# Optimization experiments

Hardware: AMD Instinct MI355X
Metric: run time of the kernel (lower is better)

Reference implementation:

```python
import math
import jax, jax.numpy as jnp
import numpy as np

B, V, D, H, DE, DFF = 2, 2048, 1024, 16, 256, 4096
DK = D // H


def setup_inputs() -> dict:
    key = jax.random.key(0)
    ks = jax.random.split(key, 24)
    n = lambda k, shape, s=0.02: (jax.random.normal(k, shape, jnp.float32) * s)
    z = lambda *shape: jnp.zeros(shape, jnp.float32)
    return {
        'x': jax.random.normal(ks[0], (B, V, D), jnp.float32),
        'e_node': jax.random.normal(ks[1], (B, V, DE), jnp.float32),
        'conn': jax.random.uniform(ks[2], (B, V, V), jnp.float32),
        'ln1_g': jnp.ones((D,), jnp.float32), 'ln1_b': z(D),
        'f1w1': n(ks[3], (DE, 2 * D)), 'f1b1': z(2 * D),
        'f1w2': n(ks[4], (2 * D, 2 * D)), 'f1b2': z(2 * D),
        'wq': n(ks[5], (D, D)), 'bq': z(D),
        'wk': n(ks[6], (D, D)), 'bk': z(D),
        'wv': n(ks[7], (D, D)), 'bv': z(D),
        'wp': n(ks[8], (D, D)), 'bp': z(D),
        'ln2_g': jnp.ones((D,), jnp.float32), 'ln2_b': z(D),
        'f2w1': n(ks[9], (DE, 2 * D)), 'f2b1': z(2 * D),
        'f2w2': n(ks[10], (2 * D, 2 * D)), 'f2b2': z(2 * D),
        'ffw1': n(ks[11], (D, DFF)), 'ffb1': z(DFF),
        'ffw2': n(ks[12], (DFF, D)), 'ffb2': z(D),
    }


def _ln(x, g, b):
    m = x.mean(-1, keepdims=True)
    v = ((x - m) ** 2).mean(-1, keepdims=True)
    return (x - m) / jnp.sqrt(v + 1e-5) * g + b


def _film(e, w1, b1, w2, b2):
    h = jax.nn.gelu(e @ w1 + b1, approximate=False)  # torch F.gelu default = exact erf
    gb = h @ w2 + b2
    return jnp.split(gb, 2, axis=-1)  # gamma, beta


def reference(x, e_node, conn, ln1_g, ln1_b, f1w1, f1b1, f1w2, f1b2,
              wq, bq, wk, bk, wv, bv, wp, bp, ln2_g, ln2_b,
              f2w1, f2b1, f2w2, f2b2, ffw1, ffb1, ffw2, ffb2):
    b, v, d = x.shape
    # Pre-norm + FiLM 1
    y = _ln(x, ln1_g, ln1_b)
    g1, be1 = _film(e_node, f1w1, f1b1, f1w2, f1b2)
    y = y * (1.0 + g1) + be1
    # Multi-head attention with additive log(conn) mask
    heads = lambda t: t.reshape(b, v, H, DK).transpose(0, 2, 1, 3)  # [B,h,V,dk]
    Q = heads(y @ wq + bq)
    K = heads(y @ wk + bk)
    Vv = heads(y @ wv + bv)
    logits = jnp.einsum('bhqd,bhkd->bhqk', Q, K) / math.sqrt(DK)
    log_mask = jnp.log(jnp.clip(conn, 0.0, 1.0) + 1e-6)[:, None]  # [B,1,V,V]
    s = logits + log_mask
    s = s - s.max(-1, keepdims=True)
    a = jnp.exp(s)
    a = a / (a.sum(-1, keepdims=True) + 1e-8)
    o = jnp.einsum('bhqk,bhkd->bhqd', a, Vv)
    o = o.transpose(0, 2, 1, 3).reshape(b, v, d)
    x = x + (o @ wp + bp)
    # Pre-norm + FiLM 2 + FFN
    y2 = _ln(x, ln2_g, ln2_b)
    g2, be2 = _film(e_node, f2w1, f2b1, f2w2, f2b2)
    y2 = y2 * (1.0 + g2) + be2
    y2 = jax.nn.gelu(y2 @ ffw1 + ffb1, approximate=False) @ ffw2 + ffb2
    return x + y2
```

## Files before the change

kernel.cpp:

```cpp
#include <hip/hip_runtime.h>
#include <math.h>
#include <stdint.h>

#define B_   2
#define V_   2048
#define D_   1024
#define H_   16
#define DK_  64
#define DE_  256
#define DFF_ 4096
#define M_   (B_*V_)
#define D2_  (2*D_)
#define D3_  (3*D_)

typedef unsigned short u16;
typedef unsigned int   u32;
typedef __bf16 bf16x8 __attribute__((ext_vector_type(8)));
typedef u16    u16x8  __attribute__((ext_vector_type(8)));
typedef u16    u16x4  __attribute__((ext_vector_type(4)));
typedef float  f32x4  __attribute__((ext_vector_type(4)));
typedef u32    u32x2  __attribute__((ext_vector_type(2)));
typedef u32    u32x4  __attribute__((ext_vector_type(4)));

__device__ __forceinline__ float bf2f(u16 u) {
    union { unsigned int i; float f; } z; z.i = ((unsigned int)u) << 16; return z.f;
}
__device__ __forceinline__ u16 f2bf(float f) {
    union { float f; unsigned int i; } z; z.f = f;
    unsigned int x = z.i;
    return (u16)((x + 0x7fffu + ((x >> 16) & 1u)) >> 16);
}
__device__ __forceinline__ float gelu_erf(float v) {
    return 0.5f * v * (1.0f + erff(v * 0.70710678118654752f));
}
__device__ __forceinline__ float ldv(const float* p) { return *p; }
__device__ __forceinline__ float ldv(const u16* p)   { return bf2f(*p); }
__device__ __forceinline__ void  stv(float* p, float v) { *p = v; }
__device__ __forceinline__ void  stv(u16* p,   float v) { *p = f2bf(v); }

__device__ __forceinline__ void gload16(const u16* g, u16* lds)
{
    __builtin_amdgcn_global_load_lds(
        (const __attribute__((address_space(1))) void*)g,
        (__attribute__((address_space(3))) void*)(uintptr_t)lds,
        16, 0, 0);
}

__device__ __forceinline__ void barrier_raw()
{
    asm volatile("" ::: "memory");
    __builtin_amdgcn_s_barrier();
    asm volatile("" ::: "memory");
}

__global__ void convT_k(const float* __restrict__ W, u16* __restrict__ Wt, int K, int N)
{
    __shared__ float tile[32][33];
    const int n0 = blockIdx.x * 32, k0 = blockIdx.y * 32;
    const int tx = threadIdx.x, ty = threadIdx.y;
    #pragma unroll
    for (int j = 0; j < 4; ++j)
        tile[ty * 4 + j][tx] = W[(size_t)(k0 + ty * 4 + j) * N + n0 + tx];
    __syncthreads();
    #pragma unroll
    for (int j = 0; j < 4; ++j)
        Wt[(size_t)(n0 + ty * 4 + j) * K + k0 + tx] = f2bf(tile[tx][ty * 4 + j]);
}

__global__ void convT3_k(const float* __restrict__ W0, const float* __restrict__ W1,
                         const float* __restrict__ W2, u16* __restrict__ Wt)
{
    __shared__ float tile[32][33];
    const float* W = blockIdx.z == 0 ? W0 : (blockIdx.z == 1 ? W1 : W2);
    u16* dst = Wt + (size_t)blockIdx.z * D_ * D_;
    const int n0 = blockIdx.x * 32, k0 = blockIdx.y * 32;
    const int tx = threadIdx.x, ty = threadIdx.y;
    #pragma unroll
    for (int j = 0; j < 4; ++j)
        tile[ty * 4 + j][tx] = W[(size_t)(k0 + ty * 4 + j) * D_ + n0 + tx];
    __syncthreads();
    #pragma unroll
    for (int j = 0; j < 4; ++j)
        dst[(size_t)(n0 + ty * 4 + j) * D_ + k0 + tx] = f2bf(tile[tx][ty * 4 + j]);
}

__global__ void conv_k(const float* __restrict__ X, u16* __restrict__ Y)
{
    const int i = (blockIdx.x * 256 + threadIdx.x) * 4;
    f32x4 v = *reinterpret_cast<const f32x4*>(X + i);
    u16x4 o;
    #pragma unroll
    for (int j = 0; j < 4; ++j) o[j] = f2bf(v[j]);
    *reinterpret_cast<u16x4*>(Y + i) = o;
}

__global__ void lmask_k(const float* __restrict__ conn, u16* __restrict__ Lm)
{
    const size_t i = ((size_t)blockIdx.x * 256 + threadIdx.x) * 8;
    f32x4 a = *reinterpret_cast<const f32x4*>(conn + i);
    f32x4 b = *reinterpret_cast<const f32x4*>(conn + i + 4);
    u16x8 o;
    #pragma unroll
    for (int j = 0; j < 4; ++j) {
        o[j]     = f2bf(__log2f(fminf(fmaxf(a[j], 0.f), 1.f) + 1e-6f));
        o[j + 4] = f2bf(__log2f(fminf(fmaxf(b[j], 0.f), 1.f) + 1e-6f));
    }
    *reinterpret_cast<u16x8*>(Lm + i) = o;
}

__global__ void qkvbias_k(const float* __restrict__ bq, const float* __restrict__ bk,
                          const float* __restrict__ bv, float* __restrict__ o)
{
    int i = blockIdx.x * 256 + threadIdx.x;
    o[i] = i < 1024 ? bq[i] : (i < 2048 ? bk[i - 1024] : bv[i - 2048]);
}

template<typename TX>
__launch_bounds__(256)
__global__ void xstats_k(const TX* __restrict__ X, float* __restrict__ stats)
{
    const int row = blockIdx.x;
    const int tid = threadIdx.x;
    const TX* xr = X + (size_t)row * D_ + tid * 4;
    float s = 0.f, sq = 0.f;
    if constexpr (sizeof(TX) == 4) {
        f32x4 v4 = *reinterpret_cast<const f32x4*>(xr);
        #pragma unroll
        for (int j = 0; j < 4; ++j) { s += v4[j]; sq += v4[j] * v4[j]; }
    } else {
        u16x4 v4 = *reinterpret_cast<const u16x4*>(xr);
        #pragma unroll
        for (int j = 0; j < 4; ++j) { float v = bf2f(v4[j]); s += v; sq += v * v; }
    }
    #pragma unroll
    for (int off = 32; off; off >>= 1) {
        s  += __shfl_xor(s, off);
        sq += __shfl_xor(sq, off);
    }
    __shared__ float rs[4], rq[4];
    const int w = tid >> 6;
    if ((tid & 63) == 0) { rs[w] = s; rq[w] = sq; }
    __syncthreads();
    if (tid == 0) {
        s  = rs[0] + rs[1] + rs[2] + rs[3];
        sq = rq[0] + rq[1] + rq[2] + rq[3];
        float mean = s * (1.0f / D_);
        float var  = sq * (1.0f / D_) - mean * mean;
        stats[row * 2]     = mean;
        stats[row * 2 + 1] = rsqrtf(fmaxf(var, 0.f) + 1e-5f);
    }
}

template<int EPI, int BN, typename TC, typename TRES>
__launch_bounds__(256)
__global__ void gemm_k(const u16* __restrict__ A, const u16* __restrict__ Wt,
                       const float* __restrict__ bias, const TRES* __restrict__ res,
                       TC* __restrict__ C, int M, int N, int K)
{
    constexpr int NB = BN / 32;
    constexpr int IB = BN / 32;
    __shared__ u16 As[2][128 * 64];
    __shared__ u16 Bs[2][BN * 64];

    const int tid  = threadIdx.x;
    const int lane = tid & 63;
    const int w    = tid >> 6;
    const int wm   = (w >> 1) * 64, wn = (w & 1) * (BN / 2);
    const int m0   = blockIdx.y * 128, n0 = blockIdx.x * BN;
    const int l15  = lane & 15, l4 = lane >> 4;
    const int rStage = lane >> 3;

    int rrA[4], ccA[4];
    #pragma unroll
    for (int i = 0; i < 4; ++i) {
        rrA[i] = w * 32 + i * 8 + rStage;
        ccA[i] = (lane & 7) ^ (rrA[i] & 7);
    }
    int rrB[IB], ccB[IB];
    #pragma unroll
    for (int i = 0; i < IB; ++i) {
        rrB[i] = w * (BN / 4) + i * 8 + rStage;
        ccB[i] = (lane & 7) ^ (rrB[i] & 7);
    }

    auto stage = [&](int kt, int dd) {
        const int k0 = kt * 64;
        #pragma unroll
        for (int i = 0; i < 4; ++i)
            gload16(A + (size_t)(m0 + rrA[i]) * K + k0 + ccA[i] * 8, &As[dd][w * 2048 + i * 512]);
        #pragma unroll
        for (int i = 0; i < IB; ++i)
            gload16(Wt + (size_t)(n0 + rrB[i]) * K + k0 + ccB[i] * 8, &Bs[dd][w * (BN * 16) + i * 512]);
    };

    f32x4 acc[4][NB] = {};
    const int NT = K / 64;

    stage(0, 0);

    for (int t = 0; t < NT; ++t) {
        const int d = t & 1;
        barrier_raw();
        if (t + 1 < NT) {
            stage(t + 1, d ^ 1);
            if constexpr (BN == 128) asm volatile("s_waitcnt vmcnt(8)" ::: "memory");
            else                     asm volatile("s_waitcnt vmcnt(6)" ::: "memory");
        } else {
            asm volatile("s_waitcnt vmcnt(0)" ::: "memory");
        }
        barrier_raw();
        __builtin_amdgcn_sched_barrier(0);

        #pragma unroll
        for (int kk = 0; kk < 2; ++kk) {
            bf16x8 a[4], b[NB];
            #pragma unroll
            for (int mb = 0; mb < 4; ++mb) {
                int r  = wm + mb * 16 + l15;
                int ph = (kk * 4 + l4) ^ (r & 7);
                a[mb] = *reinterpret_cast<const bf16x8*>(&As[d][r * 64 + ph * 8]);
            }
            #pragma unroll
            for (int nb = 0; nb < NB; ++nb) {
                int r  = wn + nb * 16 + l15;
                int ph = (kk * 4 + l4) ^ (r & 7);
                b[nb] = *reinterpret_cast<const bf16x8*>(&Bs[d][r * 64 + ph * 8]);
            }
            #pragma unroll
            for (int mb = 0; mb < 4; ++mb)
                #pragma unroll
                for (int nb = 0; nb < NB; ++nb)
                    acc[mb][nb] = __builtin_amdgcn_mfma_f32_16x16x32_bf16(a[mb], b[nb], acc[mb][nb], 0, 0, 0);
        }
    }

    #pragma unroll
    for (int nb = 0; nb < NB; ++nb) {
        int col = n0 + wn + nb * 16 + l15;
        float bv = bias[col];
        #pragma unroll
        for (int mb = 0; mb < 4; ++mb) {
            #pragma unroll
            for (int i = 0; i < 4; ++i) {
                int row = m0 + wm + mb * 16 + l4 * 4 + i;
                float v = acc[mb][nb][i] + bv;
                if (EPI == 1) v = gelu_erf(v);
                if (EPI == 2) v += ldv(res + (size_t)row * N + col);
                stv(C + (size_t)row * N + col, v);
            }
        }
    }
}

template<typename TX>
__launch_bounds__(256)
__global__ void gemmfilm_k(const u16* __restrict__ A, const u16* __restrict__ Wt,
                           const float* __restrict__ b2, const TX* __restrict__ X,
                           const float* __restrict__ stats,
                           const float* __restrict__ lng, const float* __restrict__ lnb,
                           u16* __restrict__ Y)
{
    constexpr int Kc = D2_;
    __shared__ u16 As[2][128 * 64];
    __shared__ u16 Bs[2][128 * 64];

    const int tid  = threadIdx.x;
    const int lane = tid & 63;
    const int w    = tid >> 6;
    const int wm   = (w >> 1) * 64, wn = (w & 1) * 32;
    const int m0   = blockIdx.y * 128, n0 = blockIdx.x * 64;
    const int l15  = lane & 15, l4 = lane >> 4;
    const int rStage = lane >> 3;

    int rrA[4], ccA[4];
    #pragma unroll
    for (int i = 0; i < 4; ++i) {
        rrA[i] = w * 32 + i * 8 + rStage;
        ccA[i] = (lane & 7) ^ (rrA[i] & 7);
    }
    int rowB[4], ccB[4], grB[4];
    #pragma unroll
    for (int i = 0; i < 4; ++i) {
        int lr = w * 16 + (i & 1) * 8 + rStage;
        rowB[i] = (i < 2 ? 0 : 64) + lr;
        grB[i]  = (i < 2 ? n0 : D_ + n0) + lr;
        ccB[i]  = (lane & 7) ^ (lr & 7);
    }

    auto stage = [&](int kt, int dd) {
        const int k0 = kt * 64;
        #pragma unroll
        for (int i = 0; i < 4; ++i)
            gload16(A + (size_t)(m0 + rrA[i]) * Kc + k0 + ccA[i] * 8, &As[dd][w * 2048 + i * 512]);
        #pragma unroll
        for (int i = 0; i < 4; ++i)
            gload16(Wt + (size_t)grB[i] * Kc + k0 + ccB[i] * 8,
                    &Bs[dd][((i < 2 ? 0 : 64) + w * 16 + (i & 1) * 8) * 64]);
    };

    f32x4 accG[4][2] = {}, accB2[4][2] = {};
    const int NT = Kc / 64;

    stage(0, 0);

    for (int t = 0; t < NT; ++t) {
        const int d = t & 1;
        barrier_raw();
        if (t + 1 < NT) {
            stage(t + 1, d ^ 1);
            asm volatile("s_waitcnt vmcnt(8)" ::: "memory");
        } else {
            asm volatile("s_waitcnt vmcnt(0)" ::: "memory");
        }
        barrier_raw();
        __builtin_amdgcn_sched_barrier(0);

        #pragma unroll
        for (int kk = 0; kk < 2; ++kk) {
            bf16x8 a[4], bg[2], bb[2];
            #pragma unroll
            for (int mb = 0; mb < 4; ++mb) {
                int r  = wm + mb * 16 + l15;
                int ph = (kk * 4 + l4) ^ (r & 7);
                a[mb] = *reinterpret_cast<const bf16x8*>(&As[d][r * 64 + ph * 8]);
            }
            #pragma unroll
            for (int nb = 0; nb < 2; ++nb) {
                int r  = wn + nb * 16 + l15;
                int ph = (kk * 4 + l4) ^ (r & 7);
                bg[nb] = *reinterpret_cast<const bf16x8*>(&Bs[d][r * 64 + ph * 8]);
                bb[nb] = *reinterpret_cast<const bf16x8*>(&Bs[d][(64 + r) * 64 + ph * 8]);
            }
            #pragma unroll
            for (int mb = 0; mb < 4; ++mb)
                #pragma unroll
                for (int nb = 0; nb < 2; ++nb) {
                    accG[mb][nb]  = __builtin_amdgcn_mfma_f32_16x16x32_bf16(a[mb], bg[nb], accG[mb][nb], 0, 0, 0);
                    accB2[mb][nb] = __builtin_amdgcn_mfma_f32_16x16x32_bf16(a[mb], bb[nb], accB2[mb][nb], 0, 0, 0);
                }
        }
    }

    #pragma unroll
    for (int nb = 0; nb < 2; ++nb) {
        int col = n0 + wn + nb * 16 + l15;
        float gb_ = b2[col], bb_ = b2[D_ + col];
        float lg = lng[col], lb = lnb[col];
        #pragma unroll
        for (int mb = 0; mb < 4; ++mb) {
            #pragma unroll
            for (int i = 0; i < 4; ++i) {
                int row = m0 + wm + mb * 16 + l4 * 4 + i;
                float mean = stats[row * 2], rstd = stats[row * 2 + 1];
                float xv = ldv(X + (size_t)row * D_ + col);
                float gamma = accG[mb][nb][i] + gb_;
                float beta  = accB2[mb][nb][i] + bb_;
                float v = ((xv - mean) * rstd * lg + lb) * (1.0f + gamma) + beta;
                Y[(size_t)row * D_ + col] = f2bf(v);
            }
        }
    }
}

__launch_bounds__(256)
__global__ void attn_k(const u16* __restrict__ Q, const u16* __restrict__ K,
                       const u16* __restrict__ Vv, const u16* __restrict__ Lm,
                       u16* __restrict__ O, int ld)
{
    __shared__ u16 Ks[64 * 64];
    __shared__ u16 Vs[64 * 64];
    __shared__ u16 Lms[128 * 64];
    __shared__ u16 Ps[128 * 72];

    const int blk = blockIdx.x;
    const int qt  = blk & 15;
    const int h   = (blk >> 4) & 15;
    const int b   = blk >> 8;
    const int q0  = qt * 128;
    const int tid = threadIdx.x, lane = tid & 63, w = tid >> 6;
    const int l15 = lane & 15, l4 = lane >> 4;
    const size_t bV = (size_t)b * V_;

    bf16x8 qa[2][2];
    #pragma unroll
    for (int g = 0; g < 2; ++g) {
        const u16* qp = Q + (bV + q0 + w * 32 + g * 16 + l15) * ld + h * 64;
        u16x8 r0 = *reinterpret_cast<const u16x8*>(qp + l4 * 8);
        u16x8 r1 = *reinterpret_cast<const u16x8*>(qp + 32 + l4 * 8);
        u16x8 s0, s1;
        #pragma unroll
        for (int j = 0; j < 8; ++j) {
            s0[j] = f2bf(bf2f(r0[j]) * 0.125f);
            s1[j] = f2bf(bf2f(r1[j]) * 0.125f);
        }
        union { u16x8 u; bf16x8 h; } c0, c1;
        c0.u = s0; c1.u = s1;
        qa[g][0] = c0.h; qa[g][1] = c1.h;
    }

    const int rStage = (lane >> 3);
    const int cSw    = ((lane & 7) ^ rStage) * 8;
    const int vK     = ((lane >> 5) << 2) + ((lane & 7) >> 1);
    const int vDk    = ((lane >> 3) & 3) * 16 + (lane & 1) * 8;
    const u32 vaddr  = (u32)(uintptr_t)&Vs[0] + (l4 << 10) + (l15 << 3);

    int lmOff[4];
    #pragma unroll
    for (int kb = 0; kb < 4; ++kb)
        lmOff[kb] = ((((kb << 1) | (l4 >> 1)) ^ (l15 & 7)) << 3);

    const float LOG2E = 1.44269504088896f;
    float lrp[2] = {0.f, 0.f};
    f32x4 o4[2][4] = {};

    for (int kt = 0; kt < V_ / 64; ++kt) {
        const int k0 = kt * 64;
        if (kt) __syncthreads();
        #pragma unroll
        for (int i = 0; i < 2; ++i) {
            int r  = i * 32 + w * 8 + rStage;
            int kv = i * 32 + w * 8 + vK;
            gload16(K  + (bV + k0 + r)  * ld + h * 64 + cSw, &Ks[i * 2048 + w * 512]);
            gload16(Vv + (bV + k0 + kv) * ld + h * 64 + vDk, &Vs[i * 2048 + w * 512]);
        }
        #pragma unroll
        for (int i = 0; i < 4; ++i) {
            int r = i * 32 + w * 8 + rStage;
            gload16(Lm + (bV + q0 + r) * (size_t)V_ + k0 + cSw, &Lms[i * 2048 + w * 512]);
        }
        __syncthreads();

        #pragma unroll
        for (int g = 0; g < 2; ++g) {
            f32x4 s[4];
            #pragma unroll
            for (int kb = 0; kb < 4; ++kb) {
                int row = (kb * 16 + l15) * 64;
                bf16x8 k0f = *reinterpret_cast<const bf16x8*>(&Ks[row + ((l4 ^ (l15 & 7)) * 8)]);
                bf16x8 k1f = *reinterpret_cast<const bf16x8*>(&Ks[row + (((l4 + 4) ^ (l15 & 7)) * 8)]);
                f32x4 z = {};
                z = __builtin_amdgcn_mfma_f32_16x16x32_bf16(k0f, qa[g][0], z, 0, 0, 0);
                z = __builtin_amdgcn_mfma_f32_16x16x32_bf16(k1f, qa[g][1], z, 0, 0, 0);
                s[kb] = z;
            }
            const int lmRow = w * 32 + g * 16 + l15;
            const u16* lmBase = &Lms[lmRow * 64 + (l4 & 1) * 4];
            u16* psW = &Ps[lmRow * 72 + l4 * 4];
            #pragma unroll
            for (int kb = 0; kb < 4; ++kb) {
                u16x4 lm4 = *reinterpret_cast<const u16x4*>(lmBase + lmOff[kb]);
                float p0, p1, p2, p3;
                float t0 = fmaf(s[kb][0], LOG2E, bf2f(lm4[0]));
                float t1 = fmaf(s[kb][1], LOG2E, bf2f(lm4[1]));
                float t2 = fmaf(s[kb][2], LOG2E, bf2f(lm4[2]));
                float t3 = fmaf(s[kb][3], LOG2E, bf2f(lm4[3]));
                asm("v_exp_f32 %0, %1" : "=v"(p0) : "v"(t0));
                asm("v_exp_f32 %0, %1" : "=v"(p1) : "v"(t1));
                asm("v_exp_f32 %0, %1" : "=v"(p2) : "v"(t2));
                asm("v_exp_f32 %0, %1" : "=v"(p3) : "v"(t3));
                lrp[g] += (p0 + p1) + (p2 + p3);
                u32 d0, d1;
                asm("v_cvt_pk_bf16_f32 %0, %1, %2" : "=v"(d0) : "v"(p0), "v"(p1));
                asm("v_cvt_pk_bf16_f32 %0, %1, %2" : "=v"(d1) : "v"(p2), "v"(p3));
                u32x2 dd = {d0, d1};
                *reinterpret_cast<u32x2*>(psW + kb * 16) = dd;
            }
        }

        union VU { u32x4 u; bf16x8 h; };
        VU vb[2][4];
        #pragma unroll
        for (int c2 = 0; c2 < 2; ++c2) {
            u32 a0 = vaddr + c2 * 4096;
            u32x2 t0, t1, t2, t3, t4, t5, t6, t7;
            asm volatile("ds_read_b64_tr_b16 %0, %1"            : "=v"(t0) : "v"(a0));
            asm volatile("ds_read_b64_tr_b16 %0, %1 offset:512" : "=v"(t1) : "v"(a0));
            asm volatile("ds_read_b64_tr_b16 %0, %1 offset:128" : "=v"(t2) : "v"(a0));
            asm volatile("ds_read_b64_tr_b16 %0, %1 offset:640" : "=v"(t3) : "v"(a0));
            asm volatile("ds_read_b64_tr_b16 %0, %1 offset:256" : "=v"(t4) : "v"(a0));
            asm volatile("ds_read_b64_tr_b16 %0, %1 offset:768" : "=v"(t5) : "v"(a0));
            asm volatile("ds_read_b64_tr_b16 %0, %1 offset:384" : "=v"(t6) : "v"(a0));
            asm volatile("ds_read_b64_tr_b16 %0, %1 offset:896" : "=v"(t7) : "v"(a0));
            asm volatile("s_waitcnt lgkmcnt(0)" ::: "memory");
            __builtin_amdgcn_sched_barrier(0);
            vb[c2][0].u = (u32x4){t0.x, t0.y, t1.x, t1.y};
            vb[c2][1].u = (u32x4){t2.x, t2.y, t3.x, t3.y};
            vb[c2][2].u = (u32x4){t4.x, t4.y, t5.x, t5.y};
            vb[c2][3].u = (u32x4){t6.x, t6.y, t7.x, t7.y};
        }
        #pragma unroll
        for (int g = 0; g < 2; ++g) {
            const u16* pr = &Ps[(w * 32 + g * 16 + l15) * 72];
            bf16x8 pa0 = *reinterpret_cast<const bf16x8*>(pr + l4 * 8);
            bf16x8 pa1 = *reinterpret_cast<const bf16x8*>(pr + 32 + l4 * 8);
            #pragma unroll
            for (int nb = 0; nb < 4; ++nb) {
                o4[g][nb] = __builtin_amdgcn_mfma_f32_16x16x32_bf16(pa0, vb[0][nb].h, o4[g][nb], 0, 0, 0);
                o4[g][nb] = __builtin_amdgcn_mfma_f32_16x16x32_bf16(pa1, vb[1][nb].h, o4[g][nb], 0, 0, 0);
            }
        }
    }

    #pragma unroll
    for (int g = 0; g < 2; ++g) {
        float v = lrp[g];
        v += __shfl_xor(v, 16);
        v += __shfl_xor(v, 32);
        #pragma unroll
        for (int i = 0; i < 4; ++i) {
            float lw = __shfl(v, (lane & 48) | ((l4 << 2) + i));
            float rcp = 1.0f / (lw + 1e-8f);
            int q = q0 + w * 32 + g * 16 + l4 * 4 + i;
            u16* op = O + (bV + q) * D_ + h * 64;
            #pragma unroll
            for (int nb = 0; nb < 4; ++nb)
                op[nb * 16 + l15] = f2bf(o4[g][nb][i] * rcp);
        }
    }
}

extern "C" void kernel_launch(void* const* d_in, const int* in_sizes, int n_in,
                              void* d_out, int out_size, void* d_ws, size_t ws_size,
                              hipStream_t stream)
{
    (void)in_sizes; (void)n_in; (void)out_size; (void)ws_size;
    const float* x    = (const float*)d_in[0];
    const float* e    = (const float*)d_in[1];
    const float* conn = (const float*)d_in[2];
    const float* ln1g = (const float*)d_in[3];
    const float* ln1b = (const float*)d_in[4];
    const float* f1w1 = (const float*)d_in[5];
    const float* f1b1 = (const float*)d_in[6];
    const float* f1w2 = (const float*)d_in[7];
    const float* f1b2 = (const float*)d_in[8];
    const float* wq   = (const float*)d_in[9];
    const float* bq   = (const float*)d_in[10];
    const float* wk   = (const float*)d_in[11];
    const float* bk   = (const float*)d_in[12];
    const float* wv   = (const float*)d_in[13];
    const float* bv   = (const float*)d_in[14];
    const float* wp   = (const float*)d_in[15];
    const float* bp   = (const float*)d_in[16];
    const float* ln2g = (const float*)d_in[17];
    const float* ln2b = (const float*)d_in[18];
    const float* f2w1 = (const float*)d_in[19];
    const float* f2b1 = (const float*)d_in[20];
    const float* f2w2 = (const float*)d_in[21];
    const float* f2b2 = (const float*)d_in[22];
    const float* ffw1 = (const float*)d_in[23];
    const float* ffb1 = (const float*)d_in[24];
    const float* ffw2 = (const float*)d_in[25];
    const float* ffb2 = (const float*)d_in[26];
    float* out = (float*)d_out;

    char* ws = (char*)d_ws;
    const size_t MB = 1u << 20;
    u16*   Lm    = (u16*)(ws + 0);
    u16*   e_bf  = (u16*)(ws + 16 * MB);
    u16*   h     = (u16*)(ws + 18 * MB);
    u16*   wt2   = (u16*)(ws + 34 * MB);
    float* stats = (float*)(ws + 35 * MB);
    u16*   wt8   = (u16*)(ws + 36 * MB);
    u16*   y     = (u16*)(ws + 60 * MB);
    u16*   wqkvt = (u16*)(ws + 18 * MB);
    u16*   qkv   = (u16*)(ws + 24 * MB);
    float* qkvb  = (float*)(ws + 71 * MB);
    u16*   o     = (u16*)(ws + 48 * MB);
    u16*   xnew  = (u16*)(ws + 64 * MB);
    u16*   h2    = (u16*)(ws + 18 * MB);
    u16*   y2    = (u16*)(ws + 0);
    u16*   ffw1t = (u16*)(ws + 8 * MB);
    u16*   t     = (u16*)(ws + 16 * MB);
    u16*   ffw2t = (u16*)(ws + 48 * MB);

    dim3 blk(256), tblk(32, 8);
    #define CONVT(W, WT, K, N) convT_k<<<dim3((N)/32, (K)/32), tblk, 0, stream>>>(W, WT, K, N)

    conv_k <<<(M_*DE_)/1024, blk, 0, stream>>>(e, e_bf);
    lmask_k<<<(B_*(size_t)V_*V_)/2048, blk, 0, stream>>>(conn, Lm);

    CONVT(f1w1, wt2, DE_, D2_);
    gemm_k<1, 64, u16, u16><<<dim3(D2_/64, M_/128), blk, 0, stream>>>(e_bf, wt2, f1b1, (const u16*)nullptr, h, M_, D2_, DE_);
    xstats_k<float><<<M_, blk, 0, stream>>>(x, stats);
    CONVT(f1w2, wt8, D2_, D2_);
    gemmfilm_k<float><<<dim3(D_/64, M_/128), blk, 0, stream>>>(h, wt8, f1b2, x, stats, ln1g, ln1b, y);
    convT3_k<<<dim3(D_/32, D_/32, 3), tblk, 0, stream>>>(wq, wk, wv, wqkvt);
    qkvbias_k<<<D3_/256, blk, 0, stream>>>(bq, bk, bv, qkvb);
    gemm_k<0, 128, u16, u16><<<dim3(D3_/128, M_/128), blk, 0, stream>>>(y, wqkvt, qkvb, (const u16*)nullptr, qkv, M_, D3_, D_);
    attn_k<<<B_*H_*(V_/128), blk, 0, stream>>>(qkv, qkv + 1024, qkv + 2048, Lm, o, D3_);
    CONVT(wp, wt2, D_, D_);
    gemm_k<2, 64, u16, float><<<dim3(D_/64, M_/128), blk, 0, stream>>>(o, wt2, bp, x, xnew, M_, D_, D_);
    CONVT(f2w1, wt2, DE_, D2_);
    gemm_k<1, 64, u16, u16><<<dim3(D2_/64, M_/128), blk, 0, stream>>>(e_bf, wt2, f2b1, (const u16*)nullptr, h2, M_, D2_, DE_);
    xstats_k<u16><<<M_, blk, 0, stream>>>(xnew, stats);
    CONVT(f2w2, wt8, D2_, D2_);
    gemmfilm_k<u16><<<dim3(D_/64, M_/128), blk, 0, stream>>>(h2, wt8, f2b2, xnew, stats, ln2g, ln2b, y2);
    CONVT(ffw1, ffw1t, D_, DFF_);
    gemm_k<1, 128, u16, u16><<<dim3(DFF_/128, M_/128), blk, 0, stream>>>(y2, ffw1t, ffb1, (const u16*)nullptr, t, M_, DFF_, D_);
    CONVT(ffw2, ffw2t, DFF_, D_);
    gemm_k<2, 64, float, u16><<<dim3(D_/64, M_/128), blk, 0, stream>>>(t, ffw2t, ffb2, xnew, out, M_, D_, DFF_);
    #undef CONVT
}
```

Baseline: 382.4 us.

## Double-buffer attention K/V/mask tiles and merge prep kernels into one launch

The attention kernel now keeps two shared-memory buffers for the K, V and log-mask tiles. It prefetches the next key tile while computing on the current one, using raw barriers and partial vmcnt waits, and it shrinks the P staging buffer by reusing it per 16-row group. Separately, the log-mask, e-to-bf16 conversion, layernorm row statistics and QKV bias-concat kernels are merged into one block-indexed prep kernel, which removes launch overhead. Shared memory per attention block grows, which may reduce occupancy, and the per-group reuse of Ps needs correct intra-wave ordering.

Measured after the change: 378.5 us. About the same (-1.0%).

```diff
diff --git a/kernel.cpp b/kernel.cpp
--- a/kernel.cpp
+++ b/kernel.cpp
@@ -84,35 +84,63 @@
         dst[(size_t)(n0 + ty * 4 + j) * D_ + k0 + tx] = f2bf(tile[tx][ty * 4 + j]);
 }
 
-__global__ void conv_k(const float* __restrict__ X, u16* __restrict__ Y)
-{
-    const int i = (blockIdx.x * 256 + threadIdx.x) * 4;
-    f32x4 v = *reinterpret_cast<const f32x4*>(X + i);
-    u16x4 o;
-    #pragma unroll
-    for (int j = 0; j < 4; ++j) o[j] = f2bf(v[j]);
-    *reinterpret_cast<u16x4*>(Y + i) = o;
-}
-
-__global__ void lmask_k(const float* __restrict__ conn, u16* __restrict__ Lm)
-{
-    const size_t i = ((size_t)blockIdx.x * 256 + threadIdx.x) * 8;
-    f32x4 a = *reinterpret_cast<const f32x4*>(conn + i);
-    f32x4 b = *reinterpret_cast<const f32x4*>(conn + i + 4);
-    u16x8 o;
-    #pragma unroll
-    for (int j = 0; j < 4; ++j) {
-        o[j]     = f2bf(__log2f(fminf(fmaxf(a[j], 0.f), 1.f) + 1e-6f));
-        o[j + 4] = f2bf(__log2f(fminf(fmaxf(b[j], 0.f), 1.f) + 1e-6f));
-    }
-    *reinterpret_cast<u16x8*>(Lm + i) = o;
-}
-
-__global__ void qkvbias_k(const float* __restrict__ bq, const float* __restrict__ bk,
-                          const float* __restrict__ bv, float* __restrict__ o)
-{
-    int i = blockIdx.x * 256 + threadIdx.x;
-    o[i] = i < 1024 ? bq[i] : (i < 2048 ? bk[i - 1024] : bv[i - 2048]);
+#define NL_ 4096
+#define NC_ 1024
+#define NX_ 4096
+__launch_bounds__(256)
+__global__ void prep_k(const float* __restrict__ conn, u16* __restrict__ Lm,
+                       const float* __restrict__ e, u16* __restrict__ e_bf,
+                       const float* __restrict__ X, float* __restrict__ stats,
+                       const float* __restrict__ bq, const float* __restrict__ bk,
+                       const float* __restrict__ bv, float* __restrict__ qkvb)
+{
+    __shared__ float rs[4], rq[4];
+    const int bid = blockIdx.x;
+    const int tid = threadIdx.x;
+    if (bid < NL_) {
+        const size_t i = ((size_t)bid * 256 + tid) * 8;
+        f32x4 a = *reinterpret_cast<const f32x4*>(conn + i);
+        f32x4 b = *reinterpret_cast<const f32x4*>(conn + i + 4);
+        u16x8 o;
+        #pragma unroll
+        for (int j = 0; j < 4; ++j) {
+            o[j]     = f2bf(__log2f(fminf(fmaxf(a[j], 0.f), 1.f) + 1e-6f));
+            o[j + 4] = f2bf(__log2f(fminf(fmaxf(b[j], 0.f), 1.f) + 1e-6f));
+        }
+        *reinterpret_cast<u16x8*>(Lm + i) = o;
+    } else if (bid < NL_ + NC_) {
+        const int i = ((bid - NL_) * 256 + tid) * 4;
+        f32x4 v = *reinterpret_cast<const f32x4*>(e + i);
+        u16x4 o;
+        #pragma unroll
+        for (int j = 0; j < 4; ++j) o[j] = f2bf(v[j]);
+        *reinterpret_cast<u16x4*>(e_bf + i) = o;
+    } else if (bid < NL_ + NC_ + NX_) {
+        const int row = bid - NL_ - NC_;
+        f32x4 v4 = *reinterpret_cast<const f32x4*>(X + (size_t)row * D_ + tid * 4);
+        float s = 0.f, sq = 0.f;
+        #pragma unroll
+        for (int j = 0; j < 4; ++j) { s += v4[j]; sq += v4[j] * v4[j]; }
+        #pragma unroll
+        for (int off = 32; off; off >>= 1) {
+            s  += __shfl_xor(s, off);
+            sq += __shfl_xor(sq, off);
+        }
+        const int w = tid >> 6;
+        if ((tid & 63) == 0) { rs[w] = s; rq[w] = sq; }
+        __syncthreads();
+        if (tid == 0) {
+            s  = rs[0] + rs[1] + rs[2] + rs[3];
+            sq = rq[0] + rq[1] + rq[2] + rq[3];
+            float mean = s * (1.0f / D_);
+            float var  = sq * (1.0f / D_) - mean * mean;
+            stats[row * 2]     = mean;
+            stats[row * 2 + 1] = rsqrtf(fmaxf(var, 0.f) + 1e-5f);
+        }
+    } else {
+        const int i = (bid - NL_ - NC_ - NX_) * 256 + tid;
+        qkvb[i] = i < 1024 ? bq[i] : (i < 2048 ? bk[i - 1024] : bv[i - 2048]);
+    }
 }
 
 template<typename TX>
@@ -278,11 +306,10 @@
         rrA[i] = w * 32 + i * 8 + rStage;
         ccA[i] = (lane & 7) ^ (rrA[i] & 7);
     }
-    int rowB[4], ccB[4], grB[4];
+    int ccB[4], grB[4];
     #pragma unroll
     for (int i = 0; i < 4; ++i) {
         int lr = w * 16 + (i & 1) * 8 + rStage;
-        rowB[i] = (i < 2 ? 0 : 64) + lr;
         grB[i]  = (i < 2 ? n0 : D_ + n0) + lr;
         ccB[i]  = (lane & 7) ^ (lr & 7);
     }
@@ -367,10 +394,10 @@
                        const u16* __restrict__ Vv, const u16* __restrict__ Lm,
                        u16* __restrict__ O, int ld)
 {
-    __shared__ u16 Ks[64 * 64];
-    __shared__ u16 Vs[64 * 64];
-    __shared__ u16 Lms[128 * 64];
-    __shared__ u16 Ps[128 * 72];
+    __shared__ u16 Ks[2][64 * 64];
+    __shared__ u16 Vs[2][64 * 64];
+    __shared__ u16 Lms[2][128 * 64];
+    __shared__ u16 Ps[64 * 72];
 
     const int blk = blockIdx.x;
     const int qt  = blk & 15;
@@ -402,33 +429,69 @@
     const int cSw    = ((lane & 7) ^ rStage) * 8;
     const int vK     = ((lane >> 5) << 2) + ((lane & 7) >> 1);
     const int vDk    = ((lane >> 3) & 3) * 16 + (lane & 1) * 8;
-    const u32 vaddr  = (u32)(uintptr_t)&Vs[0] + (l4 << 10) + (l15 << 3);
+    const u32 vaddr  = (u32)(uintptr_t)&Vs[0][0] + (l4 << 10) + (l15 << 3);
 
     int lmOff[4];
     #pragma unroll
     for (int kb = 0; kb < 4; ++kb)
         lmOff[kb] = ((((kb << 1) | (l4 >> 1)) ^ (l15 & 7)) << 3);
+
+    auto stage = [&](int kt, int dd) {
+        const int k0 = kt * 64;
+        #pragma unroll
+        for (int i = 0; i < 2; ++i) {
+            int r  = i * 32 + w * 8 + rStage;
+            int kv = i * 32 + w * 8 + vK;
+            gload16(K  + (bV + k0 + r)  * ld + h * 64 + cSw, &Ks[dd][i * 2048 + w * 512]);
+            gload16(Vv + (bV + k0 + kv) * ld + h * 64 + vDk, &Vs[dd][i * 2048 + w * 512]);
+        }
+        #pragma unroll
+        for (int i = 0; i < 4; ++i) {
+            int r = i * 32 + w * 8 + rStage;
+            gload16(Lm + (bV + q0 + r) * (size_t)V_ + k0 + cSw, &Lms[dd][i * 2048 + w * 512]);
+        }
+    };
 
     const float LOG2E = 1.44269504088896f;
     float lrp[2] = {0.f, 0.f};
     f32x4 o4[2][4] = {};
-
-    for (int kt = 0; kt < V_ / 64; ++kt) {
-        const int k0 = kt * 64;
-        if (kt) __syncthreads();
-        #pragma unroll
-        for (int i = 0; i < 2; ++i) {
-            int r  = i * 32 + w * 8 + rStage;
-            int kv = i * 32 + w * 8 + vK;
-            gload16(K  + (bV + k0 + r)  * ld + h * 64 + cSw, &Ks[i * 2048 + w * 512]);
-            gload16(Vv + (bV + k0 + kv) * ld + h * 64 + vDk, &Vs[i * 2048 + w * 512]);
-        }
-        #pragma unroll
-        for (int i = 0; i < 4; ++i) {
-            int r = i * 32 + w * 8 + rStage;
-            gload16(Lm + (bV + q0 + r) * (size_t)V_ + k0 + cSw, &Lms[i * 2048 + w * 512]);
-        }
-        __syncthreads();
+    const int NT = V_ / 64;
+
+    stage(0, 0);
+
+    for (int kt = 0; kt < NT; ++kt) {
+        const int d = kt & 1;
+        barrier_raw();
+        if (kt + 1 < NT) {
+            stage(kt + 1, d ^ 1);
+            asm volatile("s_waitcnt vmcnt(8)" ::: "memory");
+        } else {
+            asm volatile("s_waitcnt vmcnt(0)" ::: "memory");
+        }
+        barrier_raw();
+        __builtin_amdgcn_sched_barrier(0);
+
+        union VU { u32x4 u; bf16x8 h; };
+        VU vb[2][4];
+        #pragma unroll
+        for (int c2 = 0; c2 < 2; ++c2) {
+            u32 a0 = vaddr + d * 8192 + c2 * 4096;
+            u32x2 t0, t1, t2, t3, t4, t5, t6, t7;
+            asm volatile("ds_read_b64_tr_b16 %0, %1"            : "=v"(t0) : "v"(a0));
+            asm volatile("ds_read_b64_tr_b16 %0, %1 offset:512" : "=v"(t1) : "v"(a0));
+            asm volatile("ds_read_b64_tr_b16 %0, %1 offset:128" : "=v"(t2) : "v"(a0));
+            asm volatile("ds_read_b64_tr_b16 %0, %1 offset:640" : "=v"(t3) : "v"(a0));
+            asm volatile("ds_read_b64_tr_b16 %0, %1 offset:256" : "=v"(t4) : "v"(a0));
+            asm volatile("ds_read_b64_tr_b16 %0, %1 offset:768" : "=v"(t5) : "v"(a0));
+            asm volatile("ds_read_b64_tr_b16 %0, %1 offset:384" : "=v"(t6) : "v"(a0));
+            asm volatile("ds_read_b64_tr_b16 %0, %1 offset:896" : "=v"(t7) : "v"(a0));
+            asm volatile("s_waitcnt lgkmcnt(0)" ::: "memory");
+            __builtin_amdgcn_sched_barrier(0);
+            vb[c2][0].u = (u32x4){t0.x, t0.y, t1.x, t1.y};
+            vb[c2][1].u = (u32x4){t2.x, t2.y, t3.x, t3.y};
+            vb[c2][2].u = (u32x4){t4.x, t4.y, t5.x, t5.y};
+            vb[c2][3].u = (u32x4){t6.x, t6.y, t7.x, t7.y};
+        }
 
         #pragma unroll
         for (int g = 0; g < 2; ++g) {
@@ -436,16 +499,16 @@
             #pragma unroll
             for (int kb = 0; kb < 4; ++kb) {
                 int row = (kb * 16 + l15) * 64;
-                bf16x8 k0f = *reinterpret_cast<const bf16x8*>(&Ks[row + ((l4 ^ (l15 & 7)) * 8)]);
-                bf16x8 k1f = *reinterpret_cast<const bf16x8*>(&Ks[row + (((l4 + 4) ^ (l15 & 7)) * 8)]);
+                bf16x8 k0f = *reinterpret_cast<const bf16x8*>(&Ks[d][row + ((l4 ^ (l15 & 7)) * 8)]);
+                bf16x8 k1f = *reinterpret_cast<const bf16x8*>(&Ks[d][row + (((l4 + 4) ^ (l15 & 7)) * 8)]);
                 f32x4 z = {};
                 z = __builtin_amdgcn_mfma_f32_16x16x32_bf16(k0f, qa[g][0], z, 0, 0, 0);
                 z = __builtin_amdgcn_mfma_f32_16x16x32_bf16(k1f, qa[g][1], z, 0, 0, 0);
                 s[kb] = z;
             }
             const int lmRow = w * 32 + g * 16 + l15;
-            const u16* lmBase = &Lms[lmRow * 64 + (l4 & 1) * 4];
-            u16* psW = &Ps[lmRow * 72 + l4 * 4];
+            const u16* lmBase = &Lms[d][lmRow * 64 + (l4 & 1) * 4];
+            u16* psW = &Ps[(w * 16 + l15) * 72 + l4 * 4];
             #pragma unroll
             for (int kb = 0; kb < 4; ++kb) {
                 u16x4 lm4 = *reinterpret_cast<const u16x4*>(lmBase + lmOff[kb]);
@@ -465,32 +528,7 @@
                 u32x2 dd = {d0, d1};
                 *reinterpret_cast<u32x2*>(psW + kb * 16) = dd;
             }
-        }
-
-        union VU { u32x4 u; bf16x8 h; };
-        VU vb[2][4];
-        #pragma unroll
-        for (int c2 = 0; c2 < 2; ++c2) {
-            u32 a0 = vaddr + c2 * 4096;
-            u32x2 t0, t1, t2, t3, t4, t5, t6, t7;
-            asm volatile("ds_read_b64_tr_b16 %0, %1"            : "=v"(t0) : "v"(a0));
-            asm volatile("ds_read_b64_tr_b16 %0, %1 offset:512" : "=v"(t1) : "v"(a0));
-            asm volatile("ds_read_b64_tr_b16 %0, %1 offset:128" : "=v"(t2) : "v"(a0));
-            asm volatile("ds_read_b64_tr_b16 %0, %1 offset:640" : "=v"(t3) : "v"(a0));
-            asm volatile("ds_read_b64_tr_b16 %0, %1 offset:256" : "=v"(t4) : "v"(a0));
-            asm volatile("ds_read_b64_tr_b16 %0, %1 offset:768" : "=v"(t5) : "v"(a0));
-            asm volatile("ds_read_b64_tr_b16 %0, %1 offset:384" : "=v"(t6) : "v"(a0));
-            asm volatile("ds_read_b64_tr_b16 %0, %1 offset:896" : "=v"(t7) : "v"(a0));
-            asm volatile("s_waitcnt lgkmcnt(0)" ::: "memory");
-            __builtin_amdgcn_sched_barrier(0);
-            vb[c2][0].u = (u32x4){t0.x, t0.y, t1.x, t1.y};
-            vb[c2][1].u = (u32x4){t2.x, t2.y, t3.x, t3.y};
-            vb[c2][2].u = (u32x4){t4.x, t4.y, t5.x, t5.y};
-            vb[c2][3].u = (u32x4){t6.x, t6.y, t7.x, t7.y};
-        }
-        #pragma unroll
-        for (int g = 0; g < 2; ++g) {
-            const u16* pr = &Ps[(w * 32 + g * 16 + l15) * 72];
+            const u16* pr = &Ps[(w * 16 + l15) * 72];
             bf16x8 pa0 = *reinterpret_cast<const bf16x8*>(pr + l4 * 8);
             bf16x8 pa1 = *reinterpret_cast<const bf16x8*>(pr + 32 + l4 * 8);
             #pragma unroll
@@ -576,16 +614,13 @@
     dim3 blk(256), tblk(32, 8);
     #define CONVT(W, WT, K, N) convT_k<<<dim3((N)/32, (K)/32), tblk, 0, stream>>>(W, WT, K, N)
 
-    conv_k <<<(M_*DE_)/1024, blk, 0, stream>>>(e, e_bf);
-    lmask_k<<<(B_*(size_t)V_*V_)/2048, blk, 0, stream>>>(conn, Lm);
+    prep_k<<<NL_ + NC_ + NX_ + D3_/256, blk, 0, stream>>>(conn, Lm, e, e_bf, x, stats, bq, bk, bv, qkvb);
 
     CONVT(f1w1, wt2, DE_, D2_);
     gemm_k<1, 64, u16, u16><<<dim3(D2_/64, M_/128), blk, 0, stream>>>(e_bf, wt2, f1b1, (const u16*)nullptr, h, M_, D2_, DE_);
-    xstats_k<float><<<M_, blk, 0, stream>>>(x, stats);
     CONVT(f1w2, wt8, D2_, D2_);
     gemmfilm_k<float><<<dim3(D_/64, M_/128), blk, 0, stream>>>(h, wt8, f1b2, x, stats, ln1g, ln1b, y);
     convT3_k<<<dim3(D_/32, D_/32, 3), tblk, 0, stream>>>(wq, wk, wv, wqkvt);
-    qkvbias_k<<<D3_/256, blk, 0, stream>>>(bq, bk, bv, qkvb);
     gemm_k<0, 128, u16, u16><<<dim3(D3_/128, M_/128), blk, 0, stream>>>(y, wqkvt, qkvb, (const u16*)nullptr, qkv, M_, D3_, D_);
     attn_k<<<B_*H_*(V_/128), blk, 0, stream>>>(qkv, qkv + 1024, qkv + 2048, Lm, o, D3_);
     CONVT(wp, wt2, D_, D_);
```
